# Kernel optimization log

Measured on AMD Instinct MI355X. Metric: run time of the kernel, lower is better.

Reference implementation:

```python
import jax, jax.numpy as jnp
import numpy as np

# Synaptic (snntorch) constants: alpha = exp(-dt/tau_s), beta = exp(-dt/tau_m)
DT, TAU_S, TAU_M = 1.0, 5.0, 10.0
ALPHA = float(np.exp(-DT / TAU_S))
BETA = float(np.exp(-DT / TAU_M))
THRESH = 1.0


def heaviside(u):
    return (u > 0).astype(u.dtype)


def setup_inputs() -> dict:
    key = jax.random.key(0)
    k1, k2 = jax.random.split(key)
    T, B, D1, D2 = 128, 256, 1024, 512
    inp = jax.random.uniform(k1, (T, B, D1), dtype=jnp.float32)
    # kaiming_normal_ on [d2, d1] (fan_in = d1), then * mu (=1.0)
    w = jax.random.normal(k2, (D2, D1), dtype=jnp.float32) * np.float32(np.sqrt(2.0 / D1))
    return {"input": inp, "weight": w}


def reference(input, weight):
    T, B = input.shape[0], input.shape[1]
    D2 = weight.shape[0]
    # step i (i=1..T-1) consumes F.linear(input[i-1], W); batch all GEMMs at once
    cur = jnp.einsum('tbi,oi->tbo', input[:-1], weight)  # [T-1, B, D2]

    def step(carry, c):
        syn, mem = carry
        reset = heaviside(mem - THRESH)          # spike from previous membrane
        syn = ALPHA * syn + c                    # synaptic current decay + drive
        mem = (BETA * mem + syn) * (1.0 - reset)  # zero-reset membrane update
        spk = heaviside(mem - THRESH)
        return (syn, mem), (spk, mem, syn)

    zeros = jnp.zeros((B, D2), input.dtype)
    _, (spk, V, I) = jax.lax.scan(step, (zeros, zeros), cur)

    z0 = jnp.zeros((1, B, D2), input.dtype)  # outputs at t=0 stay zero
    output = jnp.concatenate([z0, spk], axis=0)
    V = jnp.concatenate([z0, V], axis=0)
    I = jnp.concatenate([z0, I], axis=0)
    return output, V, I
```

## Files before the change

### kernel.cpp

```cpp
#include <hip/hip_runtime.h>
#include <cstddef>
#include <cstdint>

#define TT 128
#define BB 256
#define D1 1024
#define D2 512
#define SS (BB * D2)
#define MM (127 * BB)

#define ALPHA 0.8187307530779818f
#define BETA  0.9048374180359595f

typedef _Float16 half8 __attribute__((ext_vector_type(8)));
typedef float floatx16 __attribute__((ext_vector_type(16)));

__global__ __launch_bounds__(256) void convert_w(const float* __restrict__ W,
                                                 _Float16* __restrict__ Whi,
                                                 _Float16* __restrict__ Wlo) {
    const int T = blockIdx.x * 256 + threadIdx.x;
    const int l = T & 63;
    const int ch = (T >> 6) & 15;
    const int nB = (T >> 10) & 1;
    const int kt = T >> 11;
    const int row = nB * 256 + (ch & 7) * 32 + (l & 31);
    const int k = kt * 32 + (ch >> 3) * 16 + (l >> 5) * 8;
    const float* src = W + (size_t)row * D1 + k;
    float4 w0 = *(const float4*)src;
    float4 w1 = *(const float4*)(src + 4);
    float f[8] = {w0.x, w0.y, w0.z, w0.w, w1.x, w1.y, w1.z, w1.w};
    half8 hi, lo;
#pragma unroll
    for (int j = 0; j < 8; ++j) {
        _Float16 h = (_Float16)f[j];
        hi[j] = h;
        lo[j] = (_Float16)((f[j] - (float)h) * 2048.0f);
    }
    *(half8*)(Whi + (size_t)T * 8) = hi;
    *(half8*)(Wlo + (size_t)T * 8) = lo;
}

#define AHo 0
#define ALo 4096
#define WHo 8192
#define WLo 16384
#define BUFSZ 24576

#define GLOAD16(gp, lp)                                                        \
    __builtin_amdgcn_global_load_lds(                                          \
        (const __attribute__((address_space(1))) void*)(gp),                   \
        (__attribute__((address_space(3))) void*)(lp), 16, 0, 0)

__global__ __launch_bounds__(512, 2) void gemm_mfma(const float* __restrict__ A,
                                                    const _Float16* __restrict__ Whi,
                                                    const _Float16* __restrict__ Wlo,
                                                    float* __restrict__ C) {
    __shared__ _Float16 lds[2][BUFSZ];

    const int tid = threadIdx.x;
    const int lane = tid & 63;
    const int w = tid >> 6;
    const int wm = w >> 2;
    const int wn = w & 3;
    const int nB = blockIdx.x;
    const int bm = blockIdx.y * 128;
    const int bn = nB * 256;
    const int m_ = lane & 31;
    const int q = lane >> 5;

    const int o_ = tid & 3;
    const int r0 = tid >> 2;
    const int sA = (((o_ >> 1) << 2) + (r0 >> 5)) * 512 +
                   ((o_ & 1) * 32 + (r0 & 31)) * 8;
    const float* Ab0 = A + (size_t)(bm + r0) * D1 + o_ * 8;

    const _Float16* WsrcH = Whi + (size_t)nB * 8192 + (2 * w) * 512 + lane * 8;
    const _Float16* WsrcL = Wlo + (size_t)nB * 8192 + (2 * w) * 512 + lane * 8;

    const int fA0 = (wm * 2 + 0) * 512 + lane * 8;
    const int fA1 = (wm * 2 + 1) * 512 + lane * 8;
    const int fB0 = (wn * 2 + 0) * 512 + lane * 8;
    const int fB1 = (wn * 2 + 1) * 512 + lane * 8;

    floatx16 accm[2][2], accl[2][2];
#pragma unroll
    for (int i = 0; i < 2; ++i)
#pragma unroll
        for (int j = 0; j < 2; ++j) {
            accm[i][j] = (floatx16)0.0f;
            accl[i][j] = (floatx16)0.0f;
        }

    float4 ra0, ra1;
    float4 rb0, rb1;

#define STAGE_A(BUF, F0, F1)                                                   \
    {                                                                          \
        float fv[8] = {F0.x, F0.y, F0.z, F0.w, F1.x, F1.y, F1.z, F1.w};        \
        half8 hh, ll;                                                          \
        _Pragma("unroll")                                                      \
        for (int u = 0; u < 8; ++u) {                                          \
            _Float16 hv = (_Float16)fv[u];                                     \
            hh[u] = hv;                                                        \
            ll[u] = (_Float16)((fv[u] - (float)hv) * 2048.0f);                 \
        }                                                                      \
        *(half8*)&lds[BUF][AHo + sA] = hh;                                     \
        *(half8*)&lds[BUF][ALo + sA] = ll;                                     \
    }

#define MFMA12(BUF, KS)                                                        \
    {                                                                          \
        const half8 ah0 = *(const half8*)&lds[BUF][AHo + fA0 + (KS)*2048];     \
        const half8 ah1 = *(const half8*)&lds[BUF][AHo + fA1 + (KS)*2048];     \
        const half8 al0 = *(const half8*)&lds[BUF][ALo + fA0 + (KS)*2048];     \
        const half8 al1 = *(const half8*)&lds[BUF][ALo + fA1 + (KS)*2048];     \
        const half8 bh0 = *(const half8*)&lds[BUF][WHo + fB0 + (KS)*4096];     \
        const half8 bh1 = *(const half8*)&lds[BUF][WHo + fB1 + (KS)*4096];     \
        const half8 bl0 = *(const half8*)&lds[BUF][WLo + fB0 + (KS)*4096];     \
        const half8 bl1 = *(const half8*)&lds[BUF][WLo + fB1 + (KS)*4096];     \
        accm[0][0] = __builtin_amdgcn_mfma_f32_32x32x16_f16(ah0, bh0, accm[0][0], 0, 0, 0); \
        accm[0][1] = __builtin_amdgcn_mfma_f32_32x32x16_f16(ah0, bh1, accm[0][1], 0, 0, 0); \
        accm[1][0] = __builtin_amdgcn_mfma_f32_32x32x16_f16(ah1, bh0, accm[1][0], 0, 0, 0); \
        accm[1][1] = __builtin_amdgcn_mfma_f32_32x32x16_f16(ah1, bh1, accm[1][1], 0, 0, 0); \
        accl[0][0] = __builtin_amdgcn_mfma_f32_32x32x16_f16(ah0, bl0, accl[0][0], 0, 0, 0); \
        accl[0][1] = __builtin_amdgcn_mfma_f32_32x32x16_f16(ah0, bl1, accl[0][1], 0, 0, 0); \
        accl[1][0] = __builtin_amdgcn_mfma_f32_32x32x16_f16(ah1, bl0, accl[1][0], 0, 0, 0); \
        accl[1][1] = __builtin_amdgcn_mfma_f32_32x32x16_f16(ah1, bl1, accl[1][1], 0, 0, 0); \
        accl[0][0] = __builtin_amdgcn_mfma_f32_32x32x16_f16(al0, bh0, accl[0][0], 0, 0, 0); \
        accl[0][1] = __builtin_amdgcn_mfma_f32_32x32x16_f16(al0, bh1, accl[0][1], 0, 0, 0); \
        accl[1][0] = __builtin_amdgcn_mfma_f32_32x32x16_f16(al1, bh0, accl[1][0], 0, 0, 0); \
        accl[1][1] = __builtin_amdgcn_mfma_f32_32x32x16_f16(al1, bh1, accl[1][1], 0, 0, 0); \
    }

#define BODY(JT, BUF, C0, C1, N0, N1, PREF_A, VMN)                             \
    {                                                                          \
        asm volatile("" ::: "memory");                 \
        GLOAD16(WsrcH + (size_t)((JT) + 1) * 16384,       &lds[(BUF) ^ 1][WHo + 2 * w * 512]);      \
        GLOAD16(WsrcH + (size_t)((JT) + 1) * 16384 + 512, &lds[(BUF) ^ 1][WHo + (2 * w + 1) * 512]);\
        GLOAD16(WsrcL + (size_t)((JT) + 1) * 16384,       &lds[(BUF) ^ 1][WLo + 2 * w * 512]);      \
        GLOAD16(WsrcL + (size_t)((JT) + 1) * 16384 + 512, &lds[(BUF) ^ 1][WLo + (2 * w + 1) * 512]);\
        __builtin_amdgcn_sched_barrier(0);     \
        if (PREF_A) {                                                          \
            const int kf = ((JT) + 2) * 32;                                    \
            N0 = *(const float4*)(Ab0 + kf);                                   \
            N1 = *(const float4*)(Ab0 + kf + 4);                               \
        }                                                                      \
        STAGE_A((BUF) ^ 1, C0, C1);                                            \
        __builtin_amdgcn_s_setprio(1);                                         \
        MFMA12(BUF, 0);                                                        \
        __builtin_amdgcn_s_setprio(0);                                         \
        __builtin_amdgcn_s_setprio(1);                                         \
        MFMA12(BUF, 1);                                                        \
        __builtin_amdgcn_s_setprio(0);                                         \
        asm volatile("s_waitcnt vmcnt(" #VMN ") lgkmcnt(0)" ::: "memory");     \
        __builtin_amdgcn_s_barrier();                                          \
    }

    GLOAD16(WsrcH,       &lds[0][WHo + 2 * w * 512]);
    GLOAD16(WsrcH + 512, &lds[0][WHo + (2 * w + 1) * 512]);
    GLOAD16(WsrcL,       &lds[0][WLo + 2 * w * 512]);
    GLOAD16(WsrcL + 512, &lds[0][WLo + (2 * w + 1) * 512]);
    __builtin_amdgcn_sched_barrier(0);
    ra0 = *(const float4*)(Ab0);
    ra1 = *(const float4*)(Ab0 + 4);
    rb0 = *(const float4*)(Ab0 + 32);
    rb1 = *(const float4*)(Ab0 + 36);
    STAGE_A(0, ra0, ra1);
    asm volatile("s_waitcnt vmcnt(2) lgkmcnt(0)" ::: "memory");
    __builtin_amdgcn_s_barrier();

    for (int jj = 0; jj < 30; jj += 2) {
        BODY(jj, 0, rb0, rb1, ra0, ra1, 1, 2)
        BODY(jj + 1, 1, ra0, ra1, rb0, rb1, 1, 2)
    }
    BODY(30, 0, rb0, rb1, ra0, ra1, 0, 0)
    asm volatile("" ::: "memory");
    __builtin_amdgcn_s_setprio(1);
    MFMA12(1, 0);
    __builtin_amdgcn_s_setprio(0);
    __builtin_amdgcn_s_setprio(1);
    MFMA12(1, 1);
    __builtin_amdgcn_s_setprio(0);

#undef BODY
#undef MFMA12
#undef STAGE_A

#pragma unroll
    for (int mb = 0; mb < 2; ++mb)
#pragma unroll
        for (int nb = 0; nb < 2; ++nb) {
            const int n = bn + wn * 64 + nb * 32 + m_;
#pragma unroll
            for (int reg = 0; reg < 16; ++reg) {
                const int row = (reg & 3) + 8 * (reg >> 2) + 4 * q;
                const int m = bm + wm * 64 + mb * 32 + row;
                C[(size_t)m * D2 + n] =
                    accm[mb][nb][reg] + accl[mb][nb][reg] * (1.0f / 2048.0f);
            }
        }
}

__global__ __launch_bounds__(256) void scan_kernel(float* __restrict__ out) {
    const int j = blockIdx.x * 256 + threadIdx.x;
    float* spk = out;
    float* V = out + TT * SS;
    float* I = out + 2 * TT * SS;

    spk[j] = 0.0f;
    V[j] = 0.0f;
    I[j] = 0.0f;

    float syn = 0.0f, mem = 0.0f;

#define STEP(tt, cc)                                     \
    {                                                    \
        const float reset = (mem > 1.0f) ? 1.0f : 0.0f;  \
        syn = ALPHA * syn + (cc);                        \
        mem = (BETA * mem + syn) * (1.0f - reset);       \
        const int idx = (tt) * SS + j;                   \
        spk[idx] = (mem > 1.0f) ? 1.0f : 0.0f;           \
        V[idx] = mem;                                    \
        I[idx] = syn;                                    \
    }

    float c0 = I[1 * SS + j];
    float c1 = I[2 * SS + j];
    float c2 = I[3 * SS + j];
    float c3 = I[4 * SS + j];

    int t = 1;
    for (; t <= 117; t += 4) {
        const float n0 = I[(t + 4) * SS + j];
        const float n1 = I[(t + 5) * SS + j];
        const float n2 = I[(t + 6) * SS + j];
        const float n3 = I[(t + 7) * SS + j];
        STEP(t + 0, c0);
        STEP(t + 1, c1);
        STEP(t + 2, c2);
        STEP(t + 3, c3);
        c0 = n0; c1 = n1; c2 = n2; c3 = n3;
    }
    {
        const float n0 = I[125 * SS + j];
        const float n1 = I[126 * SS + j];
        const float n2 = I[127 * SS + j];
        STEP(121, c0);
        STEP(122, c1);
        STEP(123, c2);
        STEP(124, c3);
        STEP(125, n0);
        STEP(126, n1);
        STEP(127, n2);
    }
#undef STEP
}

extern "C" void kernel_launch(void* const* d_in, const int* in_sizes, int n_in,
                              void* d_out, int out_size, void* d_ws, size_t ws_size,
                              hipStream_t stream) {
    const float* input = (const float*)d_in[0];
    const float* weight = (const float*)d_in[1];
    float* out = (float*)d_out;

    _Float16* Whi = (_Float16*)(out + SS);
    _Float16* Wlo = Whi + (size_t)D2 * D1;

    float* Cdst = out + (size_t)2 * TT * SS + SS;

    convert_w<<<dim3((D2 * D1 / 8) / 256), dim3(256), 0, stream>>>(weight, Whi, Wlo);
    gemm_mfma<<<dim3(2, MM / 128), dim3(512), 0, stream>>>(input, Whi, Wlo, Cdst);
    scan_kernel<<<dim3(SS / 256), dim3(256), 0, stream>>>(out);
}
```

Before: 387.4 us.

## Split GEMM k-tile into barrier-synced phases and deepen scan prefetch

Restructures the MFMA main loop so each k-tile runs as two phases, each with its own barrier. The weight loads go out in one phase and the A prefetch and staging in the other, with the LDS fragment reads issued before a barrier and lgkmcnt wait. This is meant to interleave memory traffic with MFMA work across waves more evenly, in exchange for twice as many barriers. Separately, the scan kernel now prefetches two groups of four timesteps ahead instead of one, to hide global-load latency in the recurrence.

Measured after the change: 384.8 us. No clear change (-0.7%).

```diff
diff --git a/kernel.cpp b/kernel.cpp
--- a/kernel.cpp
+++ b/kernel.cpp
@@ -44,7 +44,6 @@
 #define ALo 4096
 #define WHo 8192
 #define WLo 16384
-#define BUFSZ 24576
 
 #define GLOAD16(gp, lp)                                                        \
     __builtin_amdgcn_global_load_lds(                                          \
@@ -55,7 +54,7 @@
                                                     const _Float16* __restrict__ Whi,
                                                     const _Float16* __restrict__ Wlo,
                                                     float* __restrict__ C) {
-    __shared__ _Float16 lds[2][BUFSZ];
+    __shared__ _Float16 lds[2][24576];
 
     const int tid = threadIdx.x;
     const int lane = tid & 63;
@@ -108,8 +107,21 @@
         *(half8*)&lds[BUF][ALo + sA] = ll;                                     \
     }
 
-#define MFMA12(BUF, KS)                                                        \
+#define PHASE(BUF, KS, DO_W, WJT, DO_A, AJT, N0, N1, DO_ST, C0, C1, CVM)       \
     {                                                                          \
+        asm volatile("" ::: "memory");                                         \
+        if (DO_W) {                                                            \
+            GLOAD16(WsrcH + (size_t)(WJT) * 16384,       &lds[(BUF) ^ 1][WHo + 2 * w * 512]);       \
+            GLOAD16(WsrcH + (size_t)(WJT) * 16384 + 512, &lds[(BUF) ^ 1][WHo + (2 * w + 1) * 512]); \
+            GLOAD16(WsrcL + (size_t)(WJT) * 16384,       &lds[(BUF) ^ 1][WLo + 2 * w * 512]);       \
+            GLOAD16(WsrcL + (size_t)(WJT) * 16384 + 512, &lds[(BUF) ^ 1][WLo + (2 * w + 1) * 512]); \
+            __builtin_amdgcn_sched_barrier(0);                                 \
+        }                                                                      \
+        if (DO_A) {                                                            \
+            N0 = *(const float4*)(Ab0 + (AJT) * 32);                           \
+            N1 = *(const float4*)(Ab0 + (AJT) * 32 + 4);                       \
+        }                                                                      \
+        if (DO_ST) { STAGE_A((BUF) ^ 1, C0, C1); }                             \
         const half8 ah0 = *(const half8*)&lds[BUF][AHo + fA0 + (KS)*2048];     \
         const half8 ah1 = *(const half8*)&lds[BUF][AHo + fA1 + (KS)*2048];     \
         const half8 al0 = *(const half8*)&lds[BUF][ALo + fA0 + (KS)*2048];     \
@@ -118,6 +130,10 @@
         const half8 bh1 = *(const half8*)&lds[BUF][WHo + fB1 + (KS)*4096];     \
         const half8 bl0 = *(const half8*)&lds[BUF][WLo + fB0 + (KS)*4096];     \
         const half8 bl1 = *(const half8*)&lds[BUF][WLo + fB1 + (KS)*4096];     \
+        __builtin_amdgcn_s_barrier();                                          \
+        asm volatile("s_waitcnt lgkmcnt(0)" ::: "memory");                     \
+        __builtin_amdgcn_sched_barrier(0);                                     \
+        __builtin_amdgcn_s_setprio(1);                                         \
         accm[0][0] = __builtin_amdgcn_mfma_f32_32x32x16_f16(ah0, bh0, accm[0][0], 0, 0, 0); \
         accm[0][1] = __builtin_amdgcn_mfma_f32_32x32x16_f16(ah0, bh1, accm[0][1], 0, 0, 0); \
         accm[1][0] = __builtin_amdgcn_mfma_f32_32x32x16_f16(ah1, bh0, accm[1][0], 0, 0, 0); \
@@ -130,29 +146,9 @@
         accl[0][1] = __builtin_amdgcn_mfma_f32_32x32x16_f16(al0, bh1, accl[0][1], 0, 0, 0); \
         accl[1][0] = __builtin_amdgcn_mfma_f32_32x32x16_f16(al1, bh0, accl[1][0], 0, 0, 0); \
         accl[1][1] = __builtin_amdgcn_mfma_f32_32x32x16_f16(al1, bh1, accl[1][1], 0, 0, 0); \
-    }
-
-#define BODY(JT, BUF, C0, C1, N0, N1, PREF_A, VMN)                             \
-    {                                                                          \
-        asm volatile("" ::: "memory");                 \
-        GLOAD16(WsrcH + (size_t)((JT) + 1) * 16384,       &lds[(BUF) ^ 1][WHo + 2 * w * 512]);      \
-        GLOAD16(WsrcH + (size_t)((JT) + 1) * 16384 + 512, &lds[(BUF) ^ 1][WHo + (2 * w + 1) * 512]);\
-        GLOAD16(WsrcL + (size_t)((JT) + 1) * 16384,       &lds[(BUF) ^ 1][WLo + 2 * w * 512]);      \
-        GLOAD16(WsrcL + (size_t)((JT) + 1) * 16384 + 512, &lds[(BUF) ^ 1][WLo + (2 * w + 1) * 512]);\
-        __builtin_amdgcn_sched_barrier(0);     \
-        if (PREF_A) {                                                          \
-            const int kf = ((JT) + 2) * 32;                                    \
-            N0 = *(const float4*)(Ab0 + kf);                                   \
-            N1 = *(const float4*)(Ab0 + kf + 4);                               \
-        }                                                                      \
-        STAGE_A((BUF) ^ 1, C0, C1);                                            \
-        __builtin_amdgcn_s_setprio(1);                                         \
-        MFMA12(BUF, 0);                                                        \
         __builtin_amdgcn_s_setprio(0);                                         \
-        __builtin_amdgcn_s_setprio(1);                                         \
-        MFMA12(BUF, 1);                                                        \
-        __builtin_amdgcn_s_setprio(0);                                         \
-        asm volatile("s_waitcnt vmcnt(" #VMN ") lgkmcnt(0)" ::: "memory");     \
+        if ((CVM) == 2) asm volatile("s_waitcnt vmcnt(2)" ::: "memory");       \
+        else if ((CVM) == 0) asm volatile("s_waitcnt vmcnt(0)" ::: "memory");  \
         __builtin_amdgcn_s_barrier();                                          \
     }
 
@@ -165,25 +161,23 @@
     ra1 = *(const float4*)(Ab0 + 4);
     rb0 = *(const float4*)(Ab0 + 32);
     rb1 = *(const float4*)(Ab0 + 36);
+    asm volatile("s_waitcnt vmcnt(2)" ::: "memory");
     STAGE_A(0, ra0, ra1);
-    asm volatile("s_waitcnt vmcnt(2) lgkmcnt(0)" ::: "memory");
+    asm volatile("s_waitcnt lgkmcnt(0)" ::: "memory");
     __builtin_amdgcn_s_barrier();
 
-    for (int jj = 0; jj < 30; jj += 2) {
-        BODY(jj, 0, rb0, rb1, ra0, ra1, 1, 2)
-        BODY(jj + 1, 1, ra0, ra1, rb0, rb1, 1, 2)
-    }
-    BODY(30, 0, rb0, rb1, ra0, ra1, 0, 0)
-    asm volatile("" ::: "memory");
-    __builtin_amdgcn_s_setprio(1);
-    MFMA12(1, 0);
-    __builtin_amdgcn_s_setprio(0);
-    __builtin_amdgcn_s_setprio(1);
-    MFMA12(1, 1);
-    __builtin_amdgcn_s_setprio(0);
-
-#undef BODY
-#undef MFMA12
+    for (int j = 0; j < 30; j += 2) {
+        PHASE(0, 0, 1, j + 1, 0, 0, ra0, ra1, 0, ra0, ra1, -1)
+        PHASE(0, 1, 0, 0, 1, j + 2, ra0, ra1, 1, rb0, rb1, 2)
+        PHASE(1, 0, 1, j + 2, 0, 0, rb0, rb1, 0, rb0, rb1, -1)
+        PHASE(1, 1, 0, 0, 1, j + 3, rb0, rb1, 1, ra0, ra1, 2)
+    }
+    PHASE(0, 0, 1, 31, 0, 0, ra0, ra1, 0, ra0, ra1, -1)
+    PHASE(0, 1, 0, 0, 0, 0, ra0, ra1, 1, rb0, rb1, 0)
+    PHASE(1, 0, 0, 0, 0, 0, ra0, ra1, 0, ra0, ra1, -1)
+    PHASE(1, 1, 0, 0, 0, 0, ra0, ra1, 0, ra0, ra1, -1)
+
+#undef PHASE
 #undef STAGE_A
 
 #pragma unroll
@@ -228,27 +222,36 @@
     float c1 = I[2 * SS + j];
     float c2 = I[3 * SS + j];
     float c3 = I[4 * SS + j];
+    float d0 = I[5 * SS + j];
+    float d1 = I[6 * SS + j];
+    float d2 = I[7 * SS + j];
+    float d3 = I[8 * SS + j];
 
     int t = 1;
-    for (; t <= 117; t += 4) {
-        const float n0 = I[(t + 4) * SS + j];
-        const float n1 = I[(t + 5) * SS + j];
-        const float n2 = I[(t + 6) * SS + j];
-        const float n3 = I[(t + 7) * SS + j];
+    for (; t <= 113; t += 4) {
+        const float n0 = I[(t + 8) * SS + j];
+        const float n1 = I[(t + 9) * SS + j];
+        const float n2 = I[(t + 10) * SS + j];
+        const float n3 = I[(t + 11) * SS + j];
         STEP(t + 0, c0);
         STEP(t + 1, c1);
         STEP(t + 2, c2);
         STEP(t + 3, c3);
-        c0 = n0; c1 = n1; c2 = n2; c3 = n3;
+        c0 = d0; c1 = d1; c2 = d2; c3 = d3;
+        d0 = n0; d1 = n1; d2 = n2; d3 = n3;
     }
     {
         const float n0 = I[125 * SS + j];
         const float n1 = I[126 * SS + j];
         const float n2 = I[127 * SS + j];
-        STEP(121, c0);
-        STEP(122, c1);
-        STEP(123, c2);
-        STEP(124, c3);
+        STEP(117, c0);
+        STEP(118, c1);
+        STEP(119, c2);
+        STEP(120, c3);
+        STEP(121, d0);
+        STEP(122, d1);
+        STEP(123, d2);
+        STEP(124, d3);
         STEP(125, n0);
         STEP(126, n1);
         STEP(127, n2);
```
